# Optimization experiments

Hardware: AMD Instinct MI355X
Metric: run time of the kernel (lower is better)

Reference implementation:

```python
import jax, jax.numpy as jnp
import numpy as np

B, S, D = 4, 4096, 1024

def setup_inputs() -> dict:
    key = jax.random.key(0)
    kx, kq, kk, kv = jax.random.split(key, 4)
    x = jax.random.normal(kx, (B, S, D), dtype=jnp.float32)
    # nn.Linear weights, stored here as [d_in, d_out] so y = x @ W
    scale = 1.0 / np.sqrt(D)
    Wq = jax.random.normal(kq, (D, D), dtype=jnp.float32) * scale
    Wk = jax.random.normal(kk, (D, D), dtype=jnp.float32) * scale
    Wv = jax.random.normal(kv, (D, D), dtype=jnp.float32) * scale
    return {"x": x, "Wq": Wq, "Wk": Wk, "Wv": Wv}

def reference(x, Wq, Wk, Wv):
    b, n, d_in = x.shape
    d_out = Wk.shape[1]
    q = jnp.einsum('bnd,de->bne', x, Wq)
    k = jnp.einsum('bnd,de,->bne', x, Wk, 1.0)  # keys
    v = jnp.einsum('bnd,de->bne', x, Wv)
    # full causal attention: scores scaled by 1/sqrt(d_out) AFTER masking (matches source)
    scores = jnp.einsum('bqe,bke->bqk', q, k)
    causal = jnp.triu(jnp.ones((n, n), dtype=bool), k=1)  # True above diagonal -> masked
    scores = jnp.where(causal[None, :, :], -jnp.inf, scores)
    attn = jax.nn.softmax(scores / jnp.sqrt(jnp.asarray(d_out, scores.dtype)), axis=-1)
    # dropout p=0.0 (eval) -> identity
    return jnp.einsum('bqk,bke->bqe', attn, v)
```

## Files before the change

kernel.cpp:

```cpp
#include <hip/hip_runtime.h>
#include <hip/hip_bf16.h>

#define B_ 4
#define S_ 4096
#define D_ 1024
#define NT_ 32
#define PAIRS_ 528

typedef __attribute__((ext_vector_type(8))) short short8;
typedef __attribute__((ext_vector_type(4))) float f32x4;

__device__ __forceinline__ unsigned short f2bf(float f) {
    union { float f; unsigned u; } v; v.f = f;
    unsigned u = v.u;
    return (unsigned short)((u + 0x7fffu + ((u >> 16) & 1u)) >> 16);
}

__device__ __forceinline__ void gld_lds16(const unsigned short* g, unsigned short* l) {
    __builtin_amdgcn_global_load_lds((const __attribute__((address_space(1))) void*)g,
                                     (__attribute__((address_space(3))) void*)l, 16, 0, 0);
}

__device__ __forceinline__ void stage128x32(const unsigned short* gbase, size_t ld,
                                            unsigned short* ls, int tid) {
    const int r = tid >> 2;
    const int c = (tid & 3) * 8;
    unsigned short* lw = ls + tid * 8;
    gld_lds16(gbase + (size_t)r * ld + c, lw);
    gld_lds16(gbase + (size_t)(r + 64) * ld + c, lw + 2048);
}

__global__ __launch_bounds__(256) void prep_x(const float* __restrict__ x,
                                              unsigned short* __restrict__ xb) {
    size_t i = ((size_t)blockIdx.x * 256 + threadIdx.x) * 8;
    float4 a = *(const float4*)&x[i];
    float4 b = *(const float4*)&x[i + 4];
    unsigned u0 = (unsigned)f2bf(a.x) | ((unsigned)f2bf(a.y) << 16);
    unsigned u1 = (unsigned)f2bf(a.z) | ((unsigned)f2bf(a.w) << 16);
    unsigned u2 = (unsigned)f2bf(b.x) | ((unsigned)f2bf(b.y) << 16);
    unsigned u3 = (unsigned)f2bf(b.z) | ((unsigned)f2bf(b.w) << 16);
    uint4 val; val.x = u0; val.y = u1; val.z = u2; val.w = u3;
    *(uint4*)&xb[i] = val;
}

__global__ __launch_bounds__(256) void prep_w(const float* __restrict__ Wq,
                                              const float* __restrict__ Wk,
                                              const float* __restrict__ Wv,
                                              unsigned short* __restrict__ Wt) {
    __shared__ float ls[64 * 65];
    const int z = blockIdx.z;
    const float* __restrict__ W = (z == 0) ? Wq : (z == 1) ? Wk : Wv;
    unsigned short* __restrict__ Wtz = Wt + (size_t)z * D_ * D_;
    const int k0 = blockIdx.y * 64, n0 = blockIdx.x * 64;
    const int tid = threadIdx.x;
    #pragma unroll
    for (int i = 0; i < 16; ++i) {
        int lin = i * 256 + tid, r = lin >> 6, c = lin & 63;
        ls[r * 65 + c] = W[(size_t)(k0 + r) * D_ + n0 + c];
    }
    __syncthreads();
    #pragma unroll
    for (int i = 0; i < 16; ++i) {
        int lin = i * 256 + tid, r = lin >> 6, c = lin & 63;
        Wtz[(size_t)(n0 + r) * D_ + k0 + c] = f2bf(ls[c * 65 + r]);
    }
}

__global__ __launch_bounds__(512, 2) void qkv_gemm(
    const unsigned short* __restrict__ xb, const unsigned short* __restrict__ Wt,
    unsigned short* __restrict__ Q, unsigned short* __restrict__ K,
    unsigned short* __restrict__ V)
{
    __shared__ __align__(16) unsigned short lsA[2 * 256 * 64];
    __shared__ __align__(16) unsigned short lsB[2 * 256 * 64];

    const int z = blockIdx.z;
    unsigned short* __restrict__ Y = (z == 0) ? Q : (z == 1) ? K : V;
    const float scale = (z == 0) ? 0.03125f : 1.0f;

    const int lin = blockIdx.x;
    const int wg = (lin & 7) * 32 + (lin >> 3);
    const int m0 = (wg >> 2) * 256, n0 = (wg & 3) * 256;

    const int tid = threadIdx.x, lane = tid & 63, w = tid >> 6;
    const int wm = w >> 2, wn = w & 3;
    const int quad = lane >> 4, ln = lane & 15;

    const unsigned short* Ab = xb + (size_t)m0 * D_;
    const unsigned short* Bb = Wt + (size_t)z * D_ * D_ + (size_t)n0 * D_;

#define STAGE_HALF(gbase, ldsbase)                                              \
    {                                                                           \
        _Pragma("unroll")                                                       \
        for (int i_ = 0; i_ < 2; ++i_) {                                        \
            int g_ = tid + i_ * 512;                                            \
            int r_ = g_ >> 3;                                                   \
            int cg_ = (g_ & 7) ^ (r_ & 7);                                      \
            gld_lds16((gbase) + (size_t)r_ * D_ + cg_ * 8, (ldsbase) + g_ * 8); \
        }                                                                       \
    }
#define STAGE(kt, h)                                                                   \
    {                                                                                  \
        if ((h) < 2) { STAGE_HALF(Ab + (size_t)((h) * 128) * D_ + (kt) * 64,           \
                                  &lsA[(((kt) & 1) * 2 + (h)) * 8192]) }               \
        else         { STAGE_HALF(Bb + (size_t)(((h) - 2) * 128) * D_ + (kt) * 64,     \
                                  &lsB[(((kt) & 1) * 2 + ((h) - 2)) * 8192]) }         \
    }

    const unsigned short* As;
    const unsigned short* Bs;
    short8 a[4][2], b[2][2];
    f32x4 acc[8][4] = {};

#define LDA(mh)                                                                        \
    {                                                                                  \
        _Pragma("unroll")                                                              \
        for (int mf_ = 0; mf_ < 4; ++mf_) {                                            \
            _Pragma("unroll")                                                          \
            for (int ks_ = 0; ks_ < 2; ++ks_) {                                        \
                int r_ = wm * 128 + ((mh) * 4 + mf_) * 16 + ln;                        \
                int cg_ = ks_ * 4 + quad;                                              \
                a[mf_][ks_] = *(const short8*)&As[r_ * 64 + ((cg_ ^ (r_ & 7)) << 3)];  \
            }                                                                          \
        }                                                                              \
    }
#define LDB(nh)                                                                        \
    {                                                                                  \
        _Pragma("unroll")                                                              \
        for (int nf_ = 0; nf_ < 2; ++nf_) {                                            \
            _Pragma("unroll")                                                          \
            for (int ks_ = 0; ks_ < 2; ++ks_) {                                        \
                int r_ = wn * 64 + ((nh) * 2 + nf_) * 16 + ln;                         \
                int cg_ = ks_ * 4 + quad;                                              \
                b[nf_][ks_] = *(const short8*)&Bs[r_ * 64 + ((cg_ ^ (r_ & 7)) << 3)];  \
            }                                                                          \
        }                                                                              \
    }
#define MM(mh, nh)                                                                     \
    {                                                                                  \
        __builtin_amdgcn_s_setprio(1);                                                 \
        _Pragma("unroll")                                                              \
        for (int mf_ = 0; mf_ < 4; ++mf_)                                              \
            _Pragma("unroll")                                                          \
            for (int nf_ = 0; nf_ < 2; ++nf_)                                          \
                _Pragma("unroll")                                                      \
                for (int ks_ = 0; ks_ < 2; ++ks_)                                      \
                    acc[(mh) * 4 + mf_][(nh) * 2 + nf_] =                              \
                        __builtin_amdgcn_mfma_f32_16x16x32_bf16(                       \
                            a[mf_][ks_], b[nf_][ks_],                                  \
                            acc[(mh) * 4 + mf_][(nh) * 2 + nf_], 0, 0, 0);             \
        __builtin_amdgcn_s_setprio(0);                                                 \
    }
#define LGKM0 asm volatile("s_waitcnt lgkmcnt(0)" ::: "memory")
#define VM0   asm volatile("s_waitcnt vmcnt(0)" ::: "memory")
#define BAR   __builtin_amdgcn_s_barrier()
#define SB0   __builtin_amdgcn_sched_barrier(0)

    STAGE(0, 0) STAGE(0, 1) STAGE(0, 2) STAGE(0, 3)
    VM0; SB0;
    BAR; SB0;

    #pragma unroll 2
    for (int t = 0; t < 16; ++t) {
        As = lsA + (t & 1) * 16384;
        Bs = lsB + (t & 1) * 16384;
        if (t < 15) { STAGE(t + 1, 0) STAGE(t + 1, 1) STAGE(t + 1, 2) STAGE(t + 1, 3) }
        SB0;
        LDA(0) LDB(0)
        MM(0, 0)
        LDB(1)
        MM(0, 1)
        LDA(1)
        MM(1, 1)
        LDB(0)
        MM(1, 0)
        LGKM0; SB0;
        if (t < 15) {
            VM0; SB0;
            BAR; SB0;
        }
    }

#undef STAGE_HALF
#undef STAGE
#undef LDA
#undef LDB
#undef MM
#undef LGKM0
#undef VM0
#undef BAR
#undef SB0

    #pragma unroll
    for (int mf = 0; mf < 8; ++mf)
        #pragma unroll
        for (int nf = 0; nf < 4; ++nf)
            #pragma unroll
            for (int rr = 0; rr < 4; ++rr) {
                int row = m0 + wm * 128 + mf * 16 + quad * 4 + rr;
                int col = n0 + wn * 64 + nf * 16 + ln;
                Y[(size_t)row * D_ + col] = f2bf(acc[mf][nf][rr] * scale);
            }
}

__global__ __launch_bounds__(256) void vt_trans(const unsigned short* __restrict__ V,
                                                unsigned short* __restrict__ Vt) {
    __shared__ unsigned short ls[64 * 66];
    const int s0 = blockIdx.x * 64, e0 = blockIdx.y * 64, b = blockIdx.z;
    const int tid = threadIdx.x;
    const size_t base = (size_t)b * S_ * D_;
    #pragma unroll
    for (int i = 0; i < 16; ++i) {
        int lin = i * 256 + tid, r = lin >> 6, c = lin & 63;
        ls[r * 66 + c] = V[base + (size_t)(s0 + r) * D_ + e0 + c];
    }
    __syncthreads();
    const size_t baseT = (size_t)b * D_ * S_;
    #pragma unroll
    for (int i = 0; i < 16; ++i) {
        int lin = i * 256 + tid, r = lin >> 6, c = lin & 63;
        Vt[baseT + (size_t)(e0 + r) * S_ + s0 + c] = ls[c * 66 + r];
    }
}

__global__ __launch_bounds__(256) void qk_pexp(
    const unsigned short* __restrict__ Q, const unsigned short* __restrict__ K,
    unsigned short* __restrict__ P, float* __restrict__ lpart)
{
    __shared__ __align__(16) unsigned short lsA[4096];
    __shared__ __align__(16) unsigned short lsB[4096];
    __shared__ float sml[2][128];

    const int l = blockIdx.x, b = blockIdx.y;
    const int r = l & 7;
    const int s = l >> 3;
    int qt, kt;
    if (s < r + 1)            { qt = r;      kt = s; }
    else if (s < 33)          { qt = 31 - r; kt = s - (r + 1); }
    else if (s < 42 + r)      { qt = 8 + r;  kt = s - 33; }
    else                      { qt = 23 - r; kt = s - (42 + r); }
    const int p = qt * (qt + 1) / 2 + kt;

    const int q0 = qt * 128, k0 = kt * 128;
    const int tid = threadIdx.x, lane = tid & 63, w = tid >> 6;
    const int wm = w >> 1, wn = w & 1, quad = lane >> 4, ln = lane & 15;
    const size_t base = (size_t)b * S_ * D_;

    const unsigned short* Qb = Q + base + (size_t)q0 * D_;
    const unsigned short* Kb = K + base + (size_t)k0 * D_;

    f32x4 acc[4][4] = {};
    for (int et = 0; et < D_ / 32; ++et) {
        stage128x32(Qb + et * 32, D_, lsA, tid);
        stage128x32(Kb + et * 32, D_, lsB, tid);
        __syncthreads();
        short8 af[4], bfr[4];
        #pragma unroll
        for (int mf = 0; mf < 4; ++mf)
            af[mf] = *(const short8*)&lsA[(wm * 64 + mf * 16 + ln) * 32 + quad * 8];
        #pragma unroll
        for (int nf = 0; nf < 4; ++nf)
            bfr[nf] = *(const short8*)&lsB[(wn * 64 + nf * 16 + ln) * 32 + quad * 8];
        #pragma unroll
        for (int mf = 0; mf < 4; ++mf)
            #pragma unroll
            for (int nf = 0; nf < 4; ++nf)
                acc[mf][nf] = __builtin_amdgcn_mfma_f32_16x16x32_bf16(af[mf], bfr[nf], acc[mf][nf], 0, 0, 0);
        __syncthreads();
    }

    const bool diag = (kt == qt);
    unsigned short* Pt = P + ((size_t)b * PAIRS_ + p) * (128 * 128);

    #pragma unroll
    for (int mf = 0; mf < 4; ++mf)
        #pragma unroll
        for (int rr = 0; rr < 4; ++rr) {
            int rowq = wm * 64 + mf * 16 + quad * 4 + rr;
            float lsum = 0.0f;
            #pragma unroll
            for (int nf = 0; nf < 4; ++nf) {
                int ckey = wn * 64 + nf * 16 + ln;
                float sc = acc[mf][nf][rr];
                float pe = (diag && ckey > rowq) ? 0.0f : __expf(fminf(sc, 60.0f));
                Pt[rowq * 128 + ckey] = f2bf(pe);
                lsum += pe;
            }
            #pragma unroll
            for (int off = 1; off < 16; off <<= 1)
                lsum += __shfl_xor(lsum, off);
            if (ln == 0) sml[wn][rowq] = lsum;
        }
    __syncthreads();

    if (tid < 128)
        lpart[((size_t)b * PAIRS_ + p) * 128 + tid] = sml[0][tid] + sml[1][tid];
}

__global__ __launch_bounds__(128) void merge_il(const float* __restrict__ lpart,
                                                float* __restrict__ il) {
    const int qt = blockIdx.x, b = blockIdx.y;
    const int row = threadIdx.x;
    const int pbase = qt * (qt + 1) / 2;
    float l = 0.0f;
    for (int kt = 0; kt <= qt; ++kt)
        l += lpart[((size_t)b * PAIRS_ + pbase + kt) * 128 + row];
    il[(size_t)b * S_ + qt * 128 + row] = 1.0f / l;
}

__global__ __launch_bounds__(256) void pv_gemm(
    const unsigned short* __restrict__ P, const unsigned short* __restrict__ Vt,
    const float* __restrict__ il, float* __restrict__ O)
{
    __shared__ __align__(16) unsigned short lsA[4096];
    __shared__ __align__(16) unsigned short lsB[4096];

    const int l = blockIdx.x;
    const int dt = l & 7;
    const int s = l >> 3;
    const int pair = s & 15;
    const int b = s >> 4;
    const int d0 = dt * 128;
    const int tid = threadIdx.x, lane = tid & 63, w = tid >> 6;
    const int wm = w >> 1, wn = w & 1, quad = lane >> 4, ln = lane & 15;

    const unsigned short* Vtb = Vt + ((size_t)b * D_ + d0) * S_;

    #pragma unroll 1
    for (int half = 0; half < 2; ++half) {
        const int qt = half ? pair : (31 - pair);
        const int q0 = qt * 128;
        const int pbase = qt * (qt + 1) / 2;

        f32x4 acc[4][4] = {};

        #pragma unroll 1
        for (int ktile = 0; ktile <= qt; ++ktile) {
            const unsigned short* Ptile = P + ((size_t)b * PAIRS_ + pbase + ktile) * (128 * 128);
            #pragma unroll 1
            for (int sub = 0; sub < 4; ++sub) {
                stage128x32(Ptile + sub * 32, 128, lsA, tid);
                stage128x32(Vtb + ktile * 128 + sub * 32, S_, lsB, tid);
                __syncthreads();
                short8 af[4], bfr[4];
                #pragma unroll
                for (int mf = 0; mf < 4; ++mf)
                    af[mf] = *(const short8*)&lsA[(wm * 64 + mf * 16 + ln) * 32 + quad * 8];
                #pragma unroll
                for (int nf = 0; nf < 4; ++nf)
                    bfr[nf] = *(const short8*)&lsB[(wn * 64 + nf * 16 + ln) * 32 + quad * 8];
                #pragma unroll
                for (int mf = 0; mf < 4; ++mf)
                    #pragma unroll
                    for (int nf = 0; nf < 4; ++nf)
                        acc[mf][nf] = __builtin_amdgcn_mfma_f32_16x16x32_bf16(af[mf], bfr[nf], acc[mf][nf], 0, 0, 0);
                __syncthreads();
            }
        }

        #pragma unroll
        for (int mf = 0; mf < 4; ++mf) {
            float ilv[4];
            #pragma unroll
            for (int rr = 0; rr < 4; ++rr)
                ilv[rr] = il[(size_t)b * S_ + q0 + wm * 64 + mf * 16 + quad * 4 + rr];
            #pragma unroll
            for (int nf = 0; nf < 4; ++nf)
                #pragma unroll
                for (int rr = 0; rr < 4; ++rr) {
                    int rowq = q0 + wm * 64 + mf * 16 + quad * 4 + rr;
                    int col = d0 + wn * 64 + nf * 16 + ln;
                    O[((size_t)b * S_ + rowq) * D_ + col] = acc[mf][nf][rr] * ilv[rr];
                }
        }
    }
}

extern "C" void kernel_launch(void* const* d_in, const int* in_sizes, int n_in,
                              void* d_out, int out_size, void* d_ws, size_t ws_size,
                              hipStream_t stream) {
    const float* x  = (const float*)d_in[0];
    const float* Wq = (const float*)d_in[1];
    const float* Wk = (const float*)d_in[2];
    const float* Wv = (const float*)d_in[3];

    const size_t nQ = (size_t)B_ * S_ * D_;
    const size_t nP = (size_t)B_ * PAIRS_ * 128 * 128;

    unsigned short* P  = (unsigned short*)d_ws;
    unsigned short* V  = P;
    unsigned short* Q  = P + nP;
    unsigned short* K  = Q + nQ;
    unsigned short* Vt = K + nQ;
    unsigned short* xb = Vt;
    unsigned short* Wt = Vt + nQ;
    float* lpart = (float*)(Wt + (size_t)3 * D_ * D_);
    float* il    = lpart + (size_t)B_ * PAIRS_ * 128;
    float* O = (float*)d_out;

    hipLaunchKernelGGL(prep_x, dim3(8192), dim3(256), 0, stream, x, xb);
    hipLaunchKernelGGL(prep_w, dim3(16, 16, 3), dim3(256), 0, stream, Wq, Wk, Wv, Wt);
    hipLaunchKernelGGL(qkv_gemm, dim3(256, 1, 3), dim3(512), 0, stream, xb, Wt, Q, K, V);
    hipLaunchKernelGGL(vt_trans, dim3(64, 16, B_), dim3(256), 0, stream, V, Vt);
    hipLaunchKernelGGL(qk_pexp, dim3(PAIRS_, B_), dim3(256), 0, stream, Q, K, P, lpart);
    hipLaunchKernelGGL(merge_il, dim3(NT_, B_), dim3(128), 0, stream, lpart, il);
    hipLaunchKernelGGL(pv_gemm, dim3(512), dim3(256), 0, stream, P, Vt, il, O);
}
```

Baseline: 442.1 us.

## Double-buffer QK and PV GEMMs with swizzled LDS and wider K-steps

Result: faster. 429.8 us (-2.8%).

```diff
diff --git a/kernel.cpp b/kernel.cpp
--- a/kernel.cpp
+++ b/kernel.cpp
@@ -21,14 +21,10 @@
                                      (__attribute__((address_space(3))) void*)l, 16, 0, 0);
 }
 
-__device__ __forceinline__ void stage128x32(const unsigned short* gbase, size_t ld,
-                                            unsigned short* ls, int tid) {
-    const int r = tid >> 2;
-    const int c = (tid & 3) * 8;
-    unsigned short* lw = ls + tid * 8;
-    gld_lds16(gbase + (size_t)r * ld + c, lw);
-    gld_lds16(gbase + (size_t)(r + 64) * ld + c, lw + 2048);
-}
+#define LGKM0 asm volatile("s_waitcnt lgkmcnt(0)" ::: "memory")
+#define VM0   asm volatile("s_waitcnt vmcnt(0)" ::: "memory")
+#define BAR   __builtin_amdgcn_s_barrier()
+#define SB0   __builtin_amdgcn_sched_barrier(0)
 
 __global__ __launch_bounds__(256) void prep_x(const float* __restrict__ x,
                                               unsigned short* __restrict__ xb) {
@@ -151,10 +147,6 @@
                             acc[(mh) * 4 + mf_][(nh) * 2 + nf_], 0, 0, 0);             \
         __builtin_amdgcn_s_setprio(0);                                                 \
     }
-#define LGKM0 asm volatile("s_waitcnt lgkmcnt(0)" ::: "memory")
-#define VM0   asm volatile("s_waitcnt vmcnt(0)" ::: "memory")
-#define BAR   __builtin_amdgcn_s_barrier()
-#define SB0   __builtin_amdgcn_sched_barrier(0)
 
     STAGE(0, 0) STAGE(0, 1) STAGE(0, 2) STAGE(0, 3)
     VM0; SB0;
@@ -186,10 +178,6 @@
 #undef LDA
 #undef LDB
 #undef MM
-#undef LGKM0
-#undef VM0
-#undef BAR
-#undef SB0
 
     #pragma unroll
     for (int mf = 0; mf < 8; ++mf)
@@ -223,12 +211,12 @@
     }
 }
 
-__global__ __launch_bounds__(256) void qk_pexp(
+__global__ __launch_bounds__(256, 2) void qk_pexp(
     const unsigned short* __restrict__ Q, const unsigned short* __restrict__ K,
     unsigned short* __restrict__ P, float* __restrict__ lpart)
 {
-    __shared__ __align__(16) unsigned short lsA[4096];
-    __shared__ __align__(16) unsigned short lsB[4096];
+    __shared__ __align__(16) unsigned short lsA[2 * 128 * 64];
+    __shared__ __align__(16) unsigned short lsB[2 * 128 * 64];
     __shared__ float sml[2][128];
 
     const int l = blockIdx.x, b = blockIdx.y;
@@ -249,25 +237,69 @@
     const unsigned short* Qb = Q + base + (size_t)q0 * D_;
     const unsigned short* Kb = K + base + (size_t)k0 * D_;
 
+#define QK_STAGE_HALF(gbase, ldsbase)                                           \
+    {                                                                           \
+        _Pragma("unroll")                                                       \
+        for (int i_ = 0; i_ < 4; ++i_) {                                        \
+            int g_ = tid + i_ * 256;                                            \
+            int r_ = g_ >> 3;                                                   \
+            int cg_ = (g_ & 7) ^ (r_ & 7);                                      \
+            gld_lds16((gbase) + (size_t)r_ * D_ + cg_ * 8, (ldsbase) + g_ * 8); \
+        }                                                                       \
+    }
+#define QK_STAGE(t)                                                             \
+    {                                                                           \
+        QK_STAGE_HALF(Qb + (t) * 64, &lsA[((t) & 1) * 8192])                    \
+        QK_STAGE_HALF(Kb + (t) * 64, &lsB[((t) & 1) * 8192])                    \
+    }
+
+    short8 a[4][2], bfr[4][2];
     f32x4 acc[4][4] = {};
-    for (int et = 0; et < D_ / 32; ++et) {
-        stage128x32(Qb + et * 32, D_, lsA, tid);
-        stage128x32(Kb + et * 32, D_, lsB, tid);
-        __syncthreads();
-        short8 af[4], bfr[4];
+
+    QK_STAGE(0)
+    VM0; SB0;
+    BAR; SB0;
+
+    #pragma unroll 2
+    for (int t = 0; t < 16; ++t) {
+        const unsigned short* As = lsA + (t & 1) * 8192;
+        const unsigned short* Bs = lsB + (t & 1) * 8192;
+        if (t < 15) QK_STAGE(t + 1)
+        SB0;
         #pragma unroll
         for (int mf = 0; mf < 4; ++mf)
-            af[mf] = *(const short8*)&lsA[(wm * 64 + mf * 16 + ln) * 32 + quad * 8];
+            #pragma unroll
+            for (int ks = 0; ks < 2; ++ks) {
+                int rr_ = wm * 64 + mf * 16 + ln;
+                int cg_ = ks * 4 + quad;
+                a[mf][ks] = *(const short8*)&As[rr_ * 64 + ((cg_ ^ (rr_ & 7)) << 3)];
+            }
         #pragma unroll
         for (int nf = 0; nf < 4; ++nf)
-            bfr[nf] = *(const short8*)&lsB[(wn * 64 + nf * 16 + ln) * 32 + quad * 8];
+            #pragma unroll
+            for (int ks = 0; ks < 2; ++ks) {
+                int rr_ = wn * 64 + nf * 16 + ln;
+                int cg_ = ks * 4 + quad;
+                bfr[nf][ks] = *(const short8*)&Bs[rr_ * 64 + ((cg_ ^ (rr_ & 7)) << 3)];
+            }
+        __builtin_amdgcn_s_setprio(1);
         #pragma unroll
         for (int mf = 0; mf < 4; ++mf)
             #pragma unroll
             for (int nf = 0; nf < 4; ++nf)
-                acc[mf][nf] = __builtin_amdgcn_mfma_f32_16x16x32_bf16(af[mf], bfr[nf], acc[mf][nf], 0, 0, 0);
-        __syncthreads();
-    }
+                #pragma unroll
+                for (int ks = 0; ks < 2; ++ks)
+                    acc[mf][nf] = __builtin_amdgcn_mfma_f32_16x16x32_bf16(
+                        a[mf][ks], bfr[nf][ks], acc[mf][nf], 0, 0, 0);
+        __builtin_amdgcn_s_setprio(0);
+        LGKM0; SB0;
+        if (t < 15) {
+            VM0; SB0;
+            BAR; SB0;
+        }
+    }
+#undef QK_STAGE_HALF
+#undef QK_STAGE
 
     const bool diag = (kt == qt);
     unsigned short* Pt = P + ((size_t)b * PAIRS_ + p) * (128 * 128);
@@ -308,54 +340,103 @@
     il[(size_t)b * S_ + qt * 128 + row] = 1.0f / l;
 }
 
-__global__ __launch_bounds__(256) void pv_gemm(
+__global__ __launch_bounds__(512, 2) void pv_gemm(
     const unsigned short* __restrict__ P, const unsigned short* __restrict__ Vt,
     const float* __restrict__ il, float* __restrict__ O)
 {
-    __shared__ __align__(16) unsigned short lsA[4096];
-    __shared__ __align__(16) unsigned short lsB[4096];
+    __shared__ __align__(16) unsigned short lsA[2 * 128 * 64];
+    __shared__ __align__(16) unsigned short lsB[2 * 256 * 64];
 
     const int l = blockIdx.x;
-    const int dt = l & 7;
-    const int s = l >> 3;
-    const int pair = s & 15;
-    const int b = s >> 4;
-    const int d0 = dt * 128;
+    const int dt4 = l & 3;
+    const int u = l >> 2;
+    const int pair = u & 15;
+    const int b = u >> 4;
+    const int d0 = dt4 * 256;
     const int tid = threadIdx.x, lane = tid & 63, w = tid >> 6;
-    const int wm = w >> 1, wn = w & 1, quad = lane >> 4, ln = lane & 15;
+    const int wm = w >> 2, wn = w & 3, quad = lane >> 4, ln = lane & 15;
 
     const unsigned short* Vtb = Vt + ((size_t)b * D_ + d0) * S_;
+
+#define PV_STAGE_A(ptile, half, buf)                                                     \
+    {                                                                                    \
+        _Pragma("unroll")                                                                \
+        for (int i_ = 0; i_ < 2; ++i_) {                                                 \
+            int g_ = tid + i_ * 512;                                                     \
+            int r_ = g_ >> 3;                                                            \
+            int cg_ = (g_ & 7) ^ (r_ & 7);                                               \
+            gld_lds16((ptile) + (half) * 64 + (size_t)r_ * 128 + cg_ * 8,                \
+                      &lsA[(buf) * 8192] + g_ * 8);                                      \
+        }                                                                                \
+    }
+#define PV_STAGE_B(c, buf)                                                               \
+    {                                                                                    \
+        _Pragma("unroll")                                                                \
+        for (int i_ = 0; i_ < 4; ++i_) {                                                 \
+            int g_ = tid + i_ * 512;                                                     \
+            int r_ = g_ >> 3;                                                            \
+            int cg_ = (g_ & 7) ^ (r_ & 7);                                               \
+            gld_lds16(Vtb + (size_t)r_ * S_ + (c) * 64 + cg_ * 8,                        \
+                      &lsB[(buf) * 16384] + g_ * 8);                                     \
+        }                                                                                \
+    }
+
+    short8 a[4][2], bfr[4][2];
 
     #pragma unroll 1
     for (int half = 0; half < 2; ++half) {
         const int qt = half ? pair : (31 - pair);
         const int q0 = qt * 128;
         const int pbase = qt * (qt + 1) / 2;
+        const int nc = 2 * (qt + 1);
+        const unsigned short* Pbase = P + ((size_t)b * PAIRS_ + pbase) * (128 * 128);
 
         f32x4 acc[4][4] = {};
 
+        PV_STAGE_A(Pbase, 0, 0)
+        PV_STAGE_B(0, 0)
+        VM0; SB0;
+        BAR; SB0;
+
         #pragma unroll 1
-        for (int ktile = 0; ktile <= qt; ++ktile) {
-            const unsigned short* Ptile = P + ((size_t)b * PAIRS_ + pbase + ktile) * (128 * 128);
-            #pragma unroll 1
-            for (int sub = 0; sub < 4; ++sub) {
-                stage128x32(Ptile + sub * 32, 128, lsA, tid);
-                stage128x32(Vtb + ktile * 128 + sub * 32, S_, lsB, tid);
-                __syncthreads();
-                short8 af[4], bfr[4];
+        for (int c = 0; c < nc; ++c) {
+            const int buf = c & 1;
+            const unsigned short* As = lsA + buf * 8192;
+            const unsigned short* Bs = lsB + buf * 16384;
+            if (c + 1 < nc) {
+                PV_STAGE_A(Pbase + (size_t)((c + 1) >> 1) * (128 * 128), (c + 1) & 1, buf ^ 1)
+                PV_STAGE_B(c + 1, buf ^ 1)
+            }
+            SB0;
+            #pragma unroll
+            for (int mf = 0; mf < 4; ++mf)
                 #pragma unroll
-                for (int mf = 0; mf < 4; ++mf)
-                    af[mf] = *(const short8*)&lsA[(wm * 64 + mf * 16 + ln) * 32 + quad * 8];
+                for (int ks = 0; ks < 2; ++ks) {
+                    int rr_ = wm * 64 + mf * 16 + ln;
+                    int cg_ = ks * 4 + quad;
+                    a[mf][ks] = *(const short8*)&As[rr_ * 64 + ((cg_ ^ (rr_ & 7)) << 3)];
+                }
+            #pragma unroll
+            for (int nf = 0; nf < 4; ++nf)
+                #pragma unroll
+                for (int ks = 0; ks < 2; ++ks) {
+                    int rr_ = wn * 64 + nf * 16 + ln;
+                    int cg_ = ks * 4 + quad;
+                    bfr[nf][ks] = *(const short8*)&Bs[rr_ * 64 + ((cg_ ^ (rr_ & 7)) << 3)];
+                }
+            __builtin_amdgcn_s_setprio(1);
+            #pragma unroll
+            for (int mf = 0; mf < 4; ++mf)
                 #pragma unroll
                 for (int nf = 0; nf < 4; ++nf)
-                    bfr[nf] = *(const short8*)&lsB[(wn * 64 + nf * 16 + ln) * 32 + quad * 8];
-                #pragma unroll
-                for (int mf = 0; mf < 4; ++mf)
                     #pragma unroll
-                    for (int nf = 0; nf < 4; ++nf)
-                        acc[mf][nf] = __builtin_amdgcn_mfma_f32_16x16x32_bf16(af[mf], bfr[nf], acc[mf][nf], 0, 0, 0);
-                __syncthreads();
-            }
+                    for (int ks = 0; ks < 2; ++ks)
+                        acc[mf][nf] = __builtin_amdgcn_mfma_f32_16x16x32_bf16(
+                            a[mf][ks], bfr[nf][ks], acc[mf][nf], 0, 0, 0);
+            __builtin_amdgcn_s_setprio(0);
+            LGKM0; SB0;
+            VM0; SB0;
+            BAR; SB0;
         }
 
         #pragma unroll
@@ -374,6 +455,8 @@
                 }
         }
     }
+#undef PV_STAGE_A
+#undef PV_STAGE_B
 }
 
 extern "C" void kernel_launch(void* const* d_in, const int* in_sizes, int n_in,
@@ -404,5 +487,5 @@
     hipLaunchKernelGGL(vt_trans, dim3(64, 16, B_), dim3(256), 0, stream, V, Vt);
     hipLaunchKernelGGL(qk_pexp, dim3(PAIRS_, B_), dim3(256), 0, stream, Q, K, P, lpart);
     hipLaunchKernelGGL(merge_il, dim3(NT_, B_), dim3(128), 0, stream, lpart, il);
-    hipLaunchKernelGGL(pv_gemm, dim3(512), dim3(256), 0, stream, P, Vt, il, O);
-}
+    hipLaunchKernelGGL(pv_gemm, dim3(256), dim3(512), 0, stream, P, Vt, il, O);
+}
```
